# Optimization experiments

Measured on AMD Instinct MI355X. Metric: run time of the kernel, lower is better.

Reference implementation:

```python
import jax, jax.numpy as jnp
import numpy as np

N_ATOM_FEATS = 64
N_RBF = 10
N_CONV = 3
N_HIDDEN = 64
N_NODES = 50000
N_EDGES = 800000
N_GRAPHS = 512


def setup_inputs() -> dict:
    key = jax.random.key(0)
    ks = jax.random.split(key, 32)
    d = {}
    d["x_ids"] = jax.random.randint(ks[0], (N_NODES,), 0, 95)
    d["edge_index"] = jax.random.randint(ks[1], (2, N_EDGES), 0, N_NODES)
    d["edge_attr"] = jax.random.uniform(ks[2], (N_EDGES,), jnp.float32) * 6.0  # distances in [0,6)
    d["batch"] = jnp.sort(jax.random.randint(ks[3], (N_NODES,), 0, N_GRAPHS))
    # parameters
    def lin(k, fan_in, shape):
        return jax.random.normal(k, shape, jnp.float32) / np.sqrt(fan_in)
    d["emb"] = jax.random.normal(ks[4], (95, N_ATOM_FEATS), jnp.float32)
    d["blk_W1"] = lin(ks[5], N_ATOM_FEATS, (N_CONV, N_ATOM_FEATS, N_ATOM_FEATS))
    d["blk_b1"] = jnp.zeros((N_CONV, N_ATOM_FEATS), jnp.float32)
    d["blk_We"] = lin(ks[6], N_RBF, (N_CONV, N_RBF, N_ATOM_FEATS))
    d["blk_be"] = jnp.zeros((N_CONV, N_ATOM_FEATS), jnp.float32)
    d["blk_W2"] = lin(ks[7], N_ATOM_FEATS, (N_CONV, N_ATOM_FEATS, N_ATOM_FEATS))
    d["blk_b2"] = jnp.zeros((N_CONV, N_ATOM_FEATS), jnp.float32)
    d["Ws"] = lin(ks[8], N_ATOM_FEATS, (N_ATOM_FEATS, 2 * N_HIDDEN))
    d["bs"] = jnp.zeros((2 * N_HIDDEN,), jnp.float32)
    d["Wbg1"] = lin(ks[9], 2 * N_HIDDEN, (2 * N_HIDDEN, N_HIDDEN))
    d["bbg1"] = jnp.zeros((N_HIDDEN,), jnp.float32)
    d["Wbg2"] = lin(ks[10], N_HIDDEN, (N_HIDDEN, 1))
    d["bbg2"] = jnp.zeros((1,), jnp.float32)
    d["Weh1"] = lin(ks[11], 2 * N_HIDDEN, (2 * N_HIDDEN, N_HIDDEN))
    d["beh1"] = jnp.zeros((N_HIDDEN,), jnp.float32)
    d["Weh2"] = lin(ks[12], N_HIDDEN, (N_HIDDEN, 1))
    d["beh2"] = jnp.zeros((1,), jnp.float32)
    return d


def reference(x_ids, edge_index, edge_attr, batch, emb,
              blk_W1, blk_b1, blk_We, blk_be, blk_W2, blk_b2,
              Ws, bs, Wbg1, bbg1, Wbg2, bbg2, Weh1, beh1, Weh2, beh2):
    src, dst = edge_index[0], edge_index[1]
    # embedding lookup [N, F]
    x = emb[x_ids]
    # Gaussian smearing RBF: [E, n_rbf]
    offset = jnp.linspace(0.0, 6.0, N_RBF).astype(edge_attr.dtype)
    coeff = -0.5 / (offset[1] - offset[0]) ** 2
    e = jnp.exp(coeff * (edge_attr[:, None] - offset) ** 2)
    # interaction blocks (SchNet-style CFConv with residual)
    for i in range(N_CONV):
        h = x @ blk_W1[i] + blk_b1[i]                     # [N, F]
        f = e @ blk_We[i] + blk_be[i]                     # [E, F] edge filters
        m = h[src] * f                                    # [E, F] messages
        agg = jax.ops.segment_sum(m, dst, num_segments=N_NODES)
        x = x + agg @ blk_W2[i] + blk_b2[i]
        x = jax.nn.softplus(x)
    # global mean pool over graphs
    sums = jax.ops.segment_sum(x, batch, num_segments=N_GRAPHS)
    cnts = jax.ops.segment_sum(jnp.ones((x.shape[0],), x.dtype), batch, num_segments=N_GRAPHS)
    c = sums / jnp.maximum(cnts, 1.0)[:, None]
    c = jax.nn.relu(c @ Ws + bs)                          # [G, 2H]
    out_bg = jax.nn.relu(c @ Wbg1 + bbg1) @ Wbg2 + bbg2   # [G, 1]
    out_eh = jax.nn.relu(c @ Weh1 + beh1) @ Weh2 + beh2   # [G, 1]
    return (out_bg, out_eh)
```

## Files before the change

kernel.cpp:

```cpp
#include <hip/hip_runtime.h>
#include <hip/hip_fp16.h>
#include <cstddef>


__device__ __forceinline__ float softplusf(float v) {
    return fmaxf(v, 0.0f) + log1pf(__expf(-fabsf(v)));
}

#define RBF_C0 1.0f
#define RBF_C1 0.60653065971f
#define RBF_C2 0.13533528324f
#define RBF_C3 0.011108996538f
#define RBF_C4 3.3546262790e-4f
#define RBF_C5 3.7266531720e-6f
#define RBF_C6 1.5229979745e-8f
#define RBF_C7 2.2897348457e-11f
#define RBF_C8 1.2664165549e-14f
#define RBF_C9 2.5767043600e-18f

__global__ void k_hist(const int* __restrict__ dst, int* __restrict__ deg, int n_edges) {
    int e = blockIdx.x * blockDim.x + threadIdx.x;
    if (e < n_edges) atomicAdd(&deg[dst[e]], 1);
}

__global__ void k_scan1(const int* __restrict__ deg, int* __restrict__ bsum, int n) {
    __shared__ int s[256];
    int i = blockIdx.x * 256 + threadIdx.x;
    s[threadIdx.x] = (i < n) ? deg[i] : 0;
    __syncthreads();
    for (int off = 128; off > 0; off >>= 1) {
        if (threadIdx.x < off) s[threadIdx.x] += s[threadIdx.x + off];
        __syncthreads();
    }
    if (threadIdx.x == 0) bsum[blockIdx.x] = s[0];
}

__global__ void k_scan2(int* __restrict__ bsum, int nb) {
    __shared__ int s[256];
    int v = (threadIdx.x < nb) ? bsum[threadIdx.x] : 0;
    s[threadIdx.x] = v;
    __syncthreads();
    for (int off = 1; off < 256; off <<= 1) {
        int t = (threadIdx.x >= off) ? s[threadIdx.x - off] : 0;
        __syncthreads();
        s[threadIdx.x] += t;
        __syncthreads();
    }
    if (threadIdx.x < nb) bsum[threadIdx.x] = s[threadIdx.x] - v;
}

__global__ void k_scan3(const int* __restrict__ deg, const int* __restrict__ bsum,
                        int* __restrict__ off_, int* __restrict__ cursor, int n) {
    __shared__ int s[256];
    int i = blockIdx.x * 256 + threadIdx.x;
    int v = (i < n) ? deg[i] : 0;
    s[threadIdx.x] = v;
    __syncthreads();
    for (int off = 1; off < 256; off <<= 1) {
        int t = (threadIdx.x >= off) ? s[threadIdx.x - off] : 0;
        __syncthreads();
        s[threadIdx.x] += t;
        __syncthreads();
    }
    if (i < n) {
        int incl = bsum[blockIdx.x] + s[threadIdx.x];
        off_[i + 1] = incl;
        cursor[i] = incl - v;
    }
    if (i == 0) off_[0] = 0;
}

__global__ void k_scatter(const int* __restrict__ src, const int* __restrict__ dst,
                          const float* __restrict__ dist, int* __restrict__ cursor,
                          int2* __restrict__ psort, int n_edges) {
    int e = blockIdx.x * blockDim.x + threadIdx.x;
    if (e >= n_edges) return;
    int t = dst[e];
    int pos = atomicAdd(&cursor[t], 1);
    psort[pos] = make_int2(src[e], __float_as_int(dist[e]));
}

__global__ void k_gemm0(const int* __restrict__ ids, const float* __restrict__ emb,
                        const float* __restrict__ W, const float* __restrict__ bias,
                        float* __restrict__ x, __half* __restrict__ h, int n_nodes) {
    int lane = threadIdx.x & 63;
    int gw = (blockIdx.x * blockDim.x + threadIdx.x) >> 6;
    gw = __builtin_amdgcn_readfirstlane(gw);
    int nw = (gridDim.x * blockDim.x) >> 6;

    float w[64];
#pragma unroll
    for (int k = 0; k < 64; ++k) w[k] = W[k * 64 + lane];
    float bj = bias[lane];

    for (int n = gw; n < n_nodes; n += nw) {
        int id = __builtin_amdgcn_readfirstlane(ids[n]);
        const float4* xr = (const float4*)(emb + (size_t)id * 64);
        float a0 = bj, a1 = 0.f, a2 = 0.f, a3 = 0.f;
#pragma unroll
        for (int q = 0; q < 4; ++q) {
            float4 v0 = xr[4 * q + 0], v1 = xr[4 * q + 1];
            float4 v2 = xr[4 * q + 2], v3 = xr[4 * q + 3];
            a0 = fmaf(v0.x, w[16 * q + 0], a0);  a0 = fmaf(v0.y, w[16 * q + 1], a0);
            a0 = fmaf(v0.z, w[16 * q + 2], a0);  a0 = fmaf(v0.w, w[16 * q + 3], a0);
            a1 = fmaf(v1.x, w[16 * q + 4], a1);  a1 = fmaf(v1.y, w[16 * q + 5], a1);
            a1 = fmaf(v1.z, w[16 * q + 6], a1);  a1 = fmaf(v1.w, w[16 * q + 7], a1);
            a2 = fmaf(v2.x, w[16 * q + 8], a2);  a2 = fmaf(v2.y, w[16 * q + 9], a2);
            a2 = fmaf(v2.z, w[16 * q + 10], a2); a2 = fmaf(v2.w, w[16 * q + 11], a2);
            a3 = fmaf(v3.x, w[16 * q + 12], a3); a3 = fmaf(v3.y, w[16 * q + 13], a3);
            a3 = fmaf(v3.z, w[16 * q + 14], a3); a3 = fmaf(v3.w, w[16 * q + 15], a3);
        }
        x[(size_t)n * 64 + lane] = emb[(size_t)id * 64 + lane];
        h[(size_t)n * 64 + lane] = __float2half((a0 + a1) + (a2 + a3));
    }
}

__global__ void k_gemm64(const float* __restrict__ X, const float* __restrict__ W,
                         const float* __restrict__ bias, __half* __restrict__ Y, int n_nodes) {
    int lane = threadIdx.x & 63;
    int gw = (blockIdx.x * blockDim.x + threadIdx.x) >> 6;
    gw = __builtin_amdgcn_readfirstlane(gw);
    int nw = (gridDim.x * blockDim.x) >> 6;

    float w[64];
#pragma unroll
    for (int k = 0; k < 64; ++k) w[k] = W[k * 64 + lane];
    float bj = bias[lane];

    for (int n = gw; n < n_nodes; n += nw) {
        const float4* xr = (const float4*)(X + (size_t)n * 64);
        float a0 = bj, a1 = 0.f, a2 = 0.f, a3 = 0.f;
#pragma unroll
        for (int q = 0; q < 4; ++q) {
            float4 v0 = xr[4 * q + 0], v1 = xr[4 * q + 1];
            float4 v2 = xr[4 * q + 2], v3 = xr[4 * q + 3];
            a0 = fmaf(v0.x, w[16 * q + 0], a0);  a0 = fmaf(v0.y, w[16 * q + 1], a0);
            a0 = fmaf(v0.z, w[16 * q + 2], a0);  a0 = fmaf(v0.w, w[16 * q + 3], a0);
            a1 = fmaf(v1.x, w[16 * q + 4], a1);  a1 = fmaf(v1.y, w[16 * q + 5], a1);
            a1 = fmaf(v1.z, w[16 * q + 6], a1);  a1 = fmaf(v1.w, w[16 * q + 7], a1);
            a2 = fmaf(v2.x, w[16 * q + 8], a2);  a2 = fmaf(v2.y, w[16 * q + 9], a2);
            a2 = fmaf(v2.z, w[16 * q + 10], a2); a2 = fmaf(v2.w, w[16 * q + 11], a2);
            a3 = fmaf(v3.x, w[16 * q + 12], a3); a3 = fmaf(v3.y, w[16 * q + 13], a3);
            a3 = fmaf(v3.z, w[16 * q + 14], a3); a3 = fmaf(v3.w, w[16 * q + 15], a3);
        }
        Y[(size_t)n * 64 + lane] = __float2half((a0 + a1) + (a2 + a3));
    }
}

__device__ __forceinline__ float filt_d(const float wp[10], float bj, float d) {
    float A = __expf(-1.125f * d * d);
    float B = __expf(1.5f * d);
    float P = wp[9];
    P = fmaf(B, P, wp[8]); P = fmaf(B, P, wp[7]); P = fmaf(B, P, wp[6]);
    P = fmaf(B, P, wp[5]); P = fmaf(B, P, wp[4]); P = fmaf(B, P, wp[3]);
    P = fmaf(B, P, wp[2]); P = fmaf(B, P, wp[1]); P = fmaf(B, P, wp[0]);
    return fmaf(A, P, bj);
}

__global__ void k_conv(const int2* __restrict__ psort, const int* __restrict__ off,
                       const __half* __restrict__ h,
                       const float* __restrict__ We, const float* __restrict__ be,
                       const float* __restrict__ W2, const float* __restrict__ b2,
                       float* __restrict__ x, int n_nodes) {
    int lane = threadIdx.x & 63;
    int gw = (blockIdx.x * blockDim.x + threadIdx.x) >> 6;
    gw = __builtin_amdgcn_readfirstlane(gw);
    int nw = (gridDim.x * blockDim.x) >> 6;

    const float C[10] = {RBF_C0, RBF_C1, RBF_C2, RBF_C3, RBF_C4,
                         RBF_C5, RBF_C6, RBF_C7, RBF_C8, RBF_C9};
    float wp[10];
#pragma unroll
    for (int r = 0; r < 10; ++r) wp[r] = We[r * 64 + lane] * C[r];
    float bj = be[lane];
    float b2j = b2[lane];

    for (int n = gw; n < n_nodes; n += nw) {
        int k0 = off[n], k1 = off[n + 1];
        float acc = 0.0f;
        int k = k0;
        for (; k + 8 <= k1; k += 8) {
            int2 p0 = psort[k + 0], p1 = psort[k + 1], p2 = psort[k + 2], p3 = psort[k + 3];
            int2 p4 = psort[k + 4], p5 = psort[k + 5], p6 = psort[k + 6], p7 = psort[k + 7];
            float g0 = __half2float(h[(size_t)p0.x * 64 + lane]);
            float g1 = __half2float(h[(size_t)p1.x * 64 + lane]);
            float g2 = __half2float(h[(size_t)p2.x * 64 + lane]);
            float g3 = __half2float(h[(size_t)p3.x * 64 + lane]);
            float g4 = __half2float(h[(size_t)p4.x * 64 + lane]);
            float g5 = __half2float(h[(size_t)p5.x * 64 + lane]);
            float g6 = __half2float(h[(size_t)p6.x * 64 + lane]);
            float g7 = __half2float(h[(size_t)p7.x * 64 + lane]);
            acc = fmaf(g0, filt_d(wp, bj, __int_as_float(p0.y)), acc);
            acc = fmaf(g1, filt_d(wp, bj, __int_as_float(p1.y)), acc);
            acc = fmaf(g2, filt_d(wp, bj, __int_as_float(p2.y)), acc);
            acc = fmaf(g3, filt_d(wp, bj, __int_as_float(p3.y)), acc);
            acc = fmaf(g4, filt_d(wp, bj, __int_as_float(p4.y)), acc);
            acc = fmaf(g5, filt_d(wp, bj, __int_as_float(p5.y)), acc);
            acc = fmaf(g6, filt_d(wp, bj, __int_as_float(p6.y)), acc);
            acc = fmaf(g7, filt_d(wp, bj, __int_as_float(p7.y)), acc);
        }
        for (; k + 4 <= k1; k += 4) {
            int2 p0 = psort[k + 0], p1 = psort[k + 1], p2 = psort[k + 2], p3 = psort[k + 3];
            float g0 = __half2float(h[(size_t)p0.x * 64 + lane]);
            float g1 = __half2float(h[(size_t)p1.x * 64 + lane]);
            float g2 = __half2float(h[(size_t)p2.x * 64 + lane]);
            float g3 = __half2float(h[(size_t)p3.x * 64 + lane]);
            acc = fmaf(g0, filt_d(wp, bj, __int_as_float(p0.y)), acc);
            acc = fmaf(g1, filt_d(wp, bj, __int_as_float(p1.y)), acc);
            acc = fmaf(g2, filt_d(wp, bj, __int_as_float(p2.y)), acc);
            acc = fmaf(g3, filt_d(wp, bj, __int_as_float(p3.y)), acc);
        }
        for (; k < k1; ++k) {
            int2 p = psort[k];
            float g = __half2float(h[(size_t)p.x * 64 + lane]);
            acc = fmaf(g, filt_d(wp, bj, __int_as_float(p.y)), acc);
        }
        float o = b2j + x[(size_t)n * 64 + lane];
#pragma unroll 8
        for (int kk = 0; kk < 64; ++kk)
            o = fmaf(__shfl(acc, kk), W2[kk * 64 + lane], o);
        x[(size_t)n * 64 + lane] = softplusf(o);
    }
}

__global__ void k_gstart(const int* __restrict__ batch, int* __restrict__ gstart,
                         int n_nodes, int n_graphs) {
    int n = blockIdx.x * blockDim.x + threadIdx.x;
    if (n >= n_nodes) return;
    int b = batch[n];
    int prev = (n == 0) ? -1 : batch[n - 1];
    for (int g = prev + 1; g <= b; ++g) gstart[g] = n;
    if (n == n_nodes - 1)
        for (int g = b + 1; g <= n_graphs; ++g) gstart[g] = n_nodes;
}

__global__ void k_pool2(const float* __restrict__ x, const int* __restrict__ gstart,
                        float* __restrict__ c, int n_graphs) {
    __shared__ float red[256];
    int g = blockIdx.x;
    int t = threadIdx.x, j = t & 63, part = t >> 6;
    int s0 = gstart[g], s1 = gstart[g + 1];
    float acc = 0.0f;
    for (int n = s0 + part; n < s1; n += 4) acc += x[(size_t)n * 64 + j];
    red[t] = acc;
    __syncthreads();
    if (part == 0) {
        float v = red[j] + red[64 + j] + red[128 + j] + red[192 + j];
        float cnt = (float)(s1 - s0);
        c[(size_t)g * 64 + j] = v / fmaxf(cnt, 1.0f);
    }
}

__global__ void k_head(const float* __restrict__ cmean,
                       const float* __restrict__ Ws, const float* __restrict__ bs,
                       const float* __restrict__ Wbg1, const float* __restrict__ bbg1,
                       const float* __restrict__ Wbg2, const float* __restrict__ bbg2,
                       const float* __restrict__ Weh1, const float* __restrict__ beh1,
                       const float* __restrict__ Weh2, const float* __restrict__ beh2,
                       float* __restrict__ out, int n_graphs) {
    __shared__ float c[64];
    __shared__ float h1[128];
    int g = blockIdx.x;
    int t = threadIdx.x;
    if (t < 64) c[t] = cmean[(size_t)g * 64 + t];
    __syncthreads();
    float a = bs[t];
#pragma unroll 8
    for (int k = 0; k < 64; ++k) a = fmaf(c[k], Ws[k * 128 + t], a);
    h1[t] = fmaxf(a, 0.0f);
    __syncthreads();

    const float* W1p = (t < 64) ? Wbg1 : Weh1;
    const float* b1p = (t < 64) ? bbg1 : beh1;
    const float* W2p = (t < 64) ? Wbg2 : Weh2;
    float b2v = (t < 64) ? bbg2[0] : beh2[0];
    int lane = t & 63;
    float a2 = b1p[lane];
#pragma unroll 8
    for (int k = 0; k < 128; ++k) a2 = fmaf(h1[k], W1p[k * 64 + lane], a2);
    a2 = fmaxf(a2, 0.0f);
    float p = a2 * W2p[lane];
#pragma unroll
    for (int off = 32; off > 0; off >>= 1) p += __shfl_down(p, off);
    if (lane == 0) out[(t < 64 ? 0 : n_graphs) + g] = p + b2v;
}

extern "C" void kernel_launch(void* const* d_in, const int* in_sizes, int n_in,
                              void* d_out, int out_size, void* d_ws, size_t ws_size,
                              hipStream_t stream) {
    const int*   x_ids = (const int*)d_in[0];
    const int*   eidx  = (const int*)d_in[1];
    const float* eattr = (const float*)d_in[2];
    const int*   batch = (const int*)d_in[3];
    const float* emb   = (const float*)d_in[4];
    const float* W1    = (const float*)d_in[5];
    const float* b1    = (const float*)d_in[6];
    const float* We    = (const float*)d_in[7];
    const float* be    = (const float*)d_in[8];
    const float* W2    = (const float*)d_in[9];
    const float* b2    = (const float*)d_in[10];
    const float* Ws_   = (const float*)d_in[11];
    const float* bs_   = (const float*)d_in[12];
    const float* Wbg1  = (const float*)d_in[13];
    const float* bbg1  = (const float*)d_in[14];
    const float* Wbg2  = (const float*)d_in[15];
    const float* bbg2  = (const float*)d_in[16];
    const float* Weh1  = (const float*)d_in[17];
    const float* beh1  = (const float*)d_in[18];
    const float* Weh2  = (const float*)d_in[19];
    const float* beh2  = (const float*)d_in[20];

    int n_nodes  = in_sizes[0];
    int n_edges  = in_sizes[2];
    int n_graphs = out_size / 2;
    const int* src = eidx;
    const int* dst = eidx + n_edges;

    char* p = (char*)d_ws;
    float* x     = (float*)p;            p += (size_t)n_nodes * 64 * sizeof(float);
    __half* h    = (__half*)p;           p += (size_t)n_nodes * 64 * sizeof(__half);
    float* cmean = (float*)p;            p += (size_t)n_graphs * 64 * sizeof(float);
    int2* psort  = (int2*)p;             p += (size_t)n_edges * sizeof(int2);
    int* deg     = (int*)p;              p += (size_t)n_nodes * sizeof(int);
    int* off_    = (int*)p;              p += (size_t)(n_nodes + 1) * sizeof(int);
    int* cursor  = (int*)p;              p += (size_t)n_nodes * sizeof(int);
    int* bsum    = (int*)p;              p += 256 * sizeof(int);
    int* gstart  = (int*)p;              p += (size_t)(n_graphs + 1) * sizeof(int);

    float* out = (float*)d_out;

    int nb = (n_nodes + 255) / 256;

    hipMemsetAsync(deg, 0, (size_t)n_nodes * sizeof(int), stream);
    k_hist<<<(n_edges + 255) / 256, 256, 0, stream>>>(dst, deg, n_edges);
    k_scan1<<<nb, 256, 0, stream>>>(deg, bsum, n_nodes);
    k_scan2<<<1, 256, 0, stream>>>(bsum, nb);
    k_scan3<<<nb, 256, 0, stream>>>(deg, bsum, off_, cursor, n_nodes);
    k_scatter<<<(n_edges + 255) / 256, 256, 0, stream>>>(src, dst, eattr, cursor,
                                                         psort, n_edges);
    k_gstart<<<(n_nodes + 255) / 256, 256, 0, stream>>>(batch, gstart, n_nodes, n_graphs);

    k_gemm0<<<2048, 256, 0, stream>>>(x_ids, emb, W1, b1, x, h, n_nodes);
    for (int l = 0; l < 3; ++l) {
        if (l > 0)
            k_gemm64<<<2048, 256, 0, stream>>>(x, W1 + l * 64 * 64, b1 + l * 64, h, n_nodes);
        k_conv<<<4096, 256, 0, stream>>>(psort, off_, h,
                                         We + l * 10 * 64, be + l * 64,
                                         W2 + l * 64 * 64, b2 + l * 64, x, n_nodes);
    }

    k_pool2<<<n_graphs, 256, 0, stream>>>(x, gstart, cmean, n_graphs);
    k_head<<<n_graphs, 128, 0, stream>>>(cmean, Ws_, bs_, Wbg1, bbg1, Wbg2, bbg2,
                                         Weh1, beh1, Weh2, beh2, out, n_graphs);
}
```

Measured before the change: 452.5 us.

## Precompute RBF exponentials per edge, stage W2 in LDS, fuse setup and pool/head kernels

The edge scatter now computes the two exponentials of the RBF factorisation once per edge and stores them with a pre-shifted source offset in a 16-byte record. This removes per-layer exp work in the conv kernel at the cost of doubling the sorted-edge storage and its read traffic. The conv kernel stages W2 in shared memory and splits the W2 matvec into four accumulators. Histogram and graph-start computation are merged into one kernel, pool and head are merged into another, and the scan is restructured. Launch bounds and the GEMM grid sizes also change.

```diff
diff --git a/kernel.cpp b/kernel.cpp
--- a/kernel.cpp
+++ b/kernel.cpp
@@ -2,10 +2,6 @@
 #include <hip/hip_fp16.h>
 #include <cstddef>
 
-
-__device__ __forceinline__ float softplusf(float v) {
-    return fmaxf(v, 0.0f) + log1pf(__expf(-fabsf(v)));
-}
 
 #define RBF_C0 1.0f
 #define RBF_C1 0.60653065971f
@@ -18,26 +14,56 @@
 #define RBF_C8 1.2664165549e-14f
 #define RBF_C9 2.5767043600e-18f
 
-__global__ void k_hist(const int* __restrict__ dst, int* __restrict__ deg, int n_edges) {
-    int e = blockIdx.x * blockDim.x + threadIdx.x;
-    if (e < n_edges) atomicAdd(&deg[dst[e]], 1);
-}
-
-__global__ void k_scan1(const int* __restrict__ deg, int* __restrict__ bsum, int n) {
+__device__ __forceinline__ float softplusf(float v) {
+    return fmaxf(v, 0.0f) + log1pf(__expf(-fabsf(v)));
+}
+
+__device__ __forceinline__ float row_gemv(const float4* __restrict__ xr,
+                                          const float w[64], float bj) {
+    float a0 = bj, a1 = 0.f, a2 = 0.f, a3 = 0.f;
+#pragma unroll
+    for (int q = 0; q < 4; ++q) {
+        float4 v0 = xr[4 * q + 0], v1 = xr[4 * q + 1];
+        float4 v2 = xr[4 * q + 2], v3 = xr[4 * q + 3];
+        a0 = fmaf(v0.x, w[16 * q + 0], a0);  a0 = fmaf(v0.y, w[16 * q + 1], a0);
+        a0 = fmaf(v0.z, w[16 * q + 2], a0);  a0 = fmaf(v0.w, w[16 * q + 3], a0);
+        a1 = fmaf(v1.x, w[16 * q + 4], a1);  a1 = fmaf(v1.y, w[16 * q + 5], a1);
+        a1 = fmaf(v1.z, w[16 * q + 6], a1);  a1 = fmaf(v1.w, w[16 * q + 7], a1);
+        a2 = fmaf(v2.x, w[16 * q + 8], a2);  a2 = fmaf(v2.y, w[16 * q + 9], a2);
+        a2 = fmaf(v2.z, w[16 * q + 10], a2); a2 = fmaf(v2.w, w[16 * q + 11], a2);
+        a3 = fmaf(v3.x, w[16 * q + 12], a3); a3 = fmaf(v3.y, w[16 * q + 13], a3);
+        a3 = fmaf(v3.z, w[16 * q + 14], a3); a3 = fmaf(v3.w, w[16 * q + 15], a3);
+    }
+    return (a0 + a1) + (a2 + a3);
+}
+
+__device__ __forceinline__ float filt_ab(const float wp[10], float bj, float A, float B) {
+    float P = wp[9];
+    P = fmaf(B, P, wp[8]); P = fmaf(B, P, wp[7]); P = fmaf(B, P, wp[6]);
+    P = fmaf(B, P, wp[5]); P = fmaf(B, P, wp[4]); P = fmaf(B, P, wp[3]);
+    P = fmaf(B, P, wp[2]); P = fmaf(B, P, wp[1]); P = fmaf(B, P, wp[0]);
+    return fmaf(A, P, bj);
+}
+
+__global__ void k_pre(const int* __restrict__ dst, int* __restrict__ deg,
+                      const int* __restrict__ batch, int* __restrict__ gstart,
+                      int n_edges, int n_nodes, int n_graphs) {
+    int tid = blockIdx.x * blockDim.x + threadIdx.x;
+    if (tid < n_edges) atomicAdd(&deg[dst[tid]], 1);
+    if (tid < n_nodes) {
+        int b = batch[tid];
+        int prev = (tid == 0) ? -1 : batch[tid - 1];
+        for (int g = prev + 1; g <= b; ++g) gstart[g] = tid;
+        if (tid == n_nodes - 1)
+            for (int g = b + 1; g <= n_graphs; ++g) gstart[g] = n_nodes;
+    }
+}
+
+__global__ void k_scana(const int* __restrict__ deg, int* __restrict__ off_,
+                        int* __restrict__ bsum, int n) {
     __shared__ int s[256];
     int i = blockIdx.x * 256 + threadIdx.x;
-    s[threadIdx.x] = (i < n) ? deg[i] : 0;
-    __syncthreads();
-    for (int off = 128; off > 0; off >>= 1) {
-        if (threadIdx.x < off) s[threadIdx.x] += s[threadIdx.x + off];
-        __syncthreads();
-    }
-    if (threadIdx.x == 0) bsum[blockIdx.x] = s[0];
-}
-
-__global__ void k_scan2(int* __restrict__ bsum, int nb) {
-    __shared__ int s[256];
-    int v = (threadIdx.x < nb) ? bsum[threadIdx.x] : 0;
+    int v = (i < n) ? deg[i] : 0;
     s[threadIdx.x] = v;
     __syncthreads();
     for (int off = 1; off < 256; off <<= 1) {
@@ -46,14 +72,13 @@
         s[threadIdx.x] += t;
         __syncthreads();
     }
-    if (threadIdx.x < nb) bsum[threadIdx.x] = s[threadIdx.x] - v;
-}
-
-__global__ void k_scan3(const int* __restrict__ deg, const int* __restrict__ bsum,
-                        int* __restrict__ off_, int* __restrict__ cursor, int n) {
+    if (i < n) off_[i + 1] = s[threadIdx.x];
+    if (threadIdx.x == 255) bsum[blockIdx.x] = s[255];
+}
+
+__global__ void k_scanb(int* __restrict__ bsum, int nb) {
     __shared__ int s[256];
-    int i = blockIdx.x * 256 + threadIdx.x;
-    int v = (i < n) ? deg[i] : 0;
+    int v = ((int)threadIdx.x < nb) ? bsum[threadIdx.x] : 0;
     s[threadIdx.x] = v;
     __syncthreads();
     for (int off = 1; off < 256; off <<= 1) {
@@ -62,109 +87,80 @@
         s[threadIdx.x] += t;
         __syncthreads();
     }
+    if ((int)threadIdx.x < nb) bsum[threadIdx.x] = s[threadIdx.x] - v;
+}
+
+__global__ void k_scanc(const int* __restrict__ deg, const int* __restrict__ bsum,
+                        int* __restrict__ off_, int* __restrict__ cursor, int n) {
+    int i = blockIdx.x * blockDim.x + threadIdx.x;
     if (i < n) {
-        int incl = bsum[blockIdx.x] + s[threadIdx.x];
+        int incl = off_[i + 1] + bsum[i >> 8];
         off_[i + 1] = incl;
-        cursor[i] = incl - v;
+        cursor[i] = incl - deg[i];
     }
     if (i == 0) off_[0] = 0;
 }
 
 __global__ void k_scatter(const int* __restrict__ src, const int* __restrict__ dst,
                           const float* __restrict__ dist, int* __restrict__ cursor,
-                          int2* __restrict__ psort, int n_edges) {
+                          int4* __restrict__ psort, int n_edges) {
     int e = blockIdx.x * blockDim.x + threadIdx.x;
     if (e >= n_edges) return;
     int t = dst[e];
     int pos = atomicAdd(&cursor[t], 1);
-    psort[pos] = make_int2(src[e], __float_as_int(dist[e]));
-}
-
-__global__ void k_gemm0(const int* __restrict__ ids, const float* __restrict__ emb,
-                        const float* __restrict__ W, const float* __restrict__ bias,
-                        float* __restrict__ x, __half* __restrict__ h, int n_nodes) {
+    float d = dist[e];
+    float A = __expf(-1.125f * d * d);
+    float B = __expf(1.5f * d);
+    psort[pos] = make_int4(src[e] << 6, __float_as_int(A), __float_as_int(B), 0);
+}
+
+__global__ __launch_bounds__(256, 4) void k_gemm0(
+        const int* __restrict__ ids, const float* __restrict__ emb,
+        const float* __restrict__ W, const float* __restrict__ bias,
+        float* __restrict__ x, __half* __restrict__ h, int n_nodes) {
     int lane = threadIdx.x & 63;
-    int gw = (blockIdx.x * blockDim.x + threadIdx.x) >> 6;
-    gw = __builtin_amdgcn_readfirstlane(gw);
+    int gw = __builtin_amdgcn_readfirstlane((blockIdx.x * blockDim.x + threadIdx.x) >> 6);
     int nw = (gridDim.x * blockDim.x) >> 6;
-
     float w[64];
 #pragma unroll
     for (int k = 0; k < 64; ++k) w[k] = W[k * 64 + lane];
     float bj = bias[lane];
-
     for (int n = gw; n < n_nodes; n += nw) {
         int id = __builtin_amdgcn_readfirstlane(ids[n]);
-        const float4* xr = (const float4*)(emb + (size_t)id * 64);
-        float a0 = bj, a1 = 0.f, a2 = 0.f, a3 = 0.f;
-#pragma unroll
-        for (int q = 0; q < 4; ++q) {
-            float4 v0 = xr[4 * q + 0], v1 = xr[4 * q + 1];
-            float4 v2 = xr[4 * q + 2], v3 = xr[4 * q + 3];
-            a0 = fmaf(v0.x, w[16 * q + 0], a0);  a0 = fmaf(v0.y, w[16 * q + 1], a0);
-            a0 = fmaf(v0.z, w[16 * q + 2], a0);  a0 = fmaf(v0.w, w[16 * q + 3], a0);
-            a1 = fmaf(v1.x, w[16 * q + 4], a1);  a1 = fmaf(v1.y, w[16 * q + 5], a1);
-            a1 = fmaf(v1.z, w[16 * q + 6], a1);  a1 = fmaf(v1.w, w[16 * q + 7], a1);
-            a2 = fmaf(v2.x, w[16 * q + 8], a2);  a2 = fmaf(v2.y, w[16 * q + 9], a2);
-            a2 = fmaf(v2.z, w[16 * q + 10], a2); a2 = fmaf(v2.w, w[16 * q + 11], a2);
-            a3 = fmaf(v3.x, w[16 * q + 12], a3); a3 = fmaf(v3.y, w[16 * q + 13], a3);
-            a3 = fmaf(v3.z, w[16 * q + 14], a3); a3 = fmaf(v3.w, w[16 * q + 15], a3);
-        }
-        x[(size_t)n * 64 + lane] = emb[(size_t)id * 64 + lane];
-        h[(size_t)n * 64 + lane] = __float2half((a0 + a1) + (a2 + a3));
-    }
-}
-
-__global__ void k_gemm64(const float* __restrict__ X, const float* __restrict__ W,
-                         const float* __restrict__ bias, __half* __restrict__ Y, int n_nodes) {
+        const float4* xr = (const float4*)(emb + id * 64);
+        float v = row_gemv(xr, w, bj);
+        x[n * 64 + lane] = emb[id * 64 + lane];
+        h[n * 64 + lane] = __float2half(v);
+    }
+}
+
+__global__ __launch_bounds__(256, 4) void k_gemm(
+        const float* __restrict__ X, const float* __restrict__ W,
+        const float* __restrict__ bias, __half* __restrict__ Y, int n_nodes) {
     int lane = threadIdx.x & 63;
-    int gw = (blockIdx.x * blockDim.x + threadIdx.x) >> 6;
-    gw = __builtin_amdgcn_readfirstlane(gw);
+    int gw = __builtin_amdgcn_readfirstlane((blockIdx.x * blockDim.x + threadIdx.x) >> 6);
     int nw = (gridDim.x * blockDim.x) >> 6;
-
     float w[64];
 #pragma unroll
     for (int k = 0; k < 64; ++k) w[k] = W[k * 64 + lane];
     float bj = bias[lane];
-
     for (int n = gw; n < n_nodes; n += nw) {
-        const float4* xr = (const float4*)(X + (size_t)n * 64);
-        float a0 = bj, a1 = 0.f, a2 = 0.f, a3 = 0.f;
-#pragma unroll
-        for (int q = 0; q < 4; ++q) {
-            float4 v0 = xr[4 * q + 0], v1 = xr[4 * q + 1];
-            float4 v2 = xr[4 * q + 2], v3 = xr[4 * q + 3];
-            a0 = fmaf(v0.x, w[16 * q + 0], a0);  a0 = fmaf(v0.y, w[16 * q + 1], a0);
-            a0 = fmaf(v0.z, w[16 * q + 2], a0);  a0 = fmaf(v0.w, w[16 * q + 3], a0);
-            a1 = fmaf(v1.x, w[16 * q + 4], a1);  a1 = fmaf(v1.y, w[16 * q + 5], a1);
-            a1 = fmaf(v1.z, w[16 * q + 6], a1);  a1 = fmaf(v1.w, w[16 * q + 7], a1);
-            a2 = fmaf(v2.x, w[16 * q + 8], a2);  a2 = fmaf(v2.y, w[16 * q + 9], a2);
-            a2 = fmaf(v2.z, w[16 * q + 10], a2); a2 = fmaf(v2.w, w[16 * q + 11], a2);
-            a3 = fmaf(v3.x, w[16 * q + 12], a3); a3 = fmaf(v3.y, w[16 * q + 13], a3);
-            a3 = fmaf(v3.z, w[16 * q + 14], a3); a3 = fmaf(v3.w, w[16 * q + 15], a3);
-        }
-        Y[(size_t)n * 64 + lane] = __float2half((a0 + a1) + (a2 + a3));
-    }
-}
-
-__device__ __forceinline__ float filt_d(const float wp[10], float bj, float d) {
-    float A = __expf(-1.125f * d * d);
-    float B = __expf(1.5f * d);
-    float P = wp[9];
-    P = fmaf(B, P, wp[8]); P = fmaf(B, P, wp[7]); P = fmaf(B, P, wp[6]);
-    P = fmaf(B, P, wp[5]); P = fmaf(B, P, wp[4]); P = fmaf(B, P, wp[3]);
-    P = fmaf(B, P, wp[2]); P = fmaf(B, P, wp[1]); P = fmaf(B, P, wp[0]);
-    return fmaf(A, P, bj);
-}
-
-__global__ void k_conv(const int2* __restrict__ psort, const int* __restrict__ off,
-                       const __half* __restrict__ h,
-                       const float* __restrict__ We, const float* __restrict__ be,
-                       const float* __restrict__ W2, const float* __restrict__ b2,
-                       float* __restrict__ x, int n_nodes) {
+        const float4* xr = (const float4*)(X + n * 64);
+        Y[n * 64 + lane] = __float2half(row_gemv(xr, w, bj));
+    }
+}
+
+__global__ __launch_bounds__(256, 4) void k_conv(
+        const int4* __restrict__ ps, const int* __restrict__ off,
+        const __half* __restrict__ h,
+        const float* __restrict__ We, const float* __restrict__ be,
+        const float* __restrict__ W2, const float* __restrict__ b2,
+        float* __restrict__ x, int n_nodes) {
+    __shared__ float sW2[4096];
+    for (int i = threadIdx.x; i < 4096; i += 256) sW2[i] = W2[i];
+
     int lane = threadIdx.x & 63;
-    int gw = (blockIdx.x * blockDim.x + threadIdx.x) >> 6;
-    gw = __builtin_amdgcn_readfirstlane(gw);
+    int gw = __builtin_amdgcn_readfirstlane((blockIdx.x * blockDim.x + threadIdx.x) >> 6);
     int nw = (gridDim.x * blockDim.x) >> 6;
 
     const float C[10] = {RBF_C0, RBF_C1, RBF_C2, RBF_C3, RBF_C4,
@@ -172,117 +168,106 @@
     float wp[10];
 #pragma unroll
     for (int r = 0; r < 10; ++r) wp[r] = We[r * 64 + lane] * C[r];
-    float bj = be[lane];
+    float bj  = be[lane];
     float b2j = b2[lane];
+    __syncthreads();
 
     for (int n = gw; n < n_nodes; n += nw) {
         int k0 = off[n], k1 = off[n + 1];
         float acc = 0.0f;
         int k = k0;
         for (; k + 8 <= k1; k += 8) {
-            int2 p0 = psort[k + 0], p1 = psort[k + 1], p2 = psort[k + 2], p3 = psort[k + 3];
-            int2 p4 = psort[k + 4], p5 = psort[k + 5], p6 = psort[k + 6], p7 = psort[k + 7];
-            float g0 = __half2float(h[(size_t)p0.x * 64 + lane]);
-            float g1 = __half2float(h[(size_t)p1.x * 64 + lane]);
-            float g2 = __half2float(h[(size_t)p2.x * 64 + lane]);
-            float g3 = __half2float(h[(size_t)p3.x * 64 + lane]);
-            float g4 = __half2float(h[(size_t)p4.x * 64 + lane]);
-            float g5 = __half2float(h[(size_t)p5.x * 64 + lane]);
-            float g6 = __half2float(h[(size_t)p6.x * 64 + lane]);
-            float g7 = __half2float(h[(size_t)p7.x * 64 + lane]);
-            acc = fmaf(g0, filt_d(wp, bj, __int_as_float(p0.y)), acc);
-            acc = fmaf(g1, filt_d(wp, bj, __int_as_float(p1.y)), acc);
-            acc = fmaf(g2, filt_d(wp, bj, __int_as_float(p2.y)), acc);
-            acc = fmaf(g3, filt_d(wp, bj, __int_as_float(p3.y)), acc);
-            acc = fmaf(g4, filt_d(wp, bj, __int_as_float(p4.y)), acc);
-            acc = fmaf(g5, filt_d(wp, bj, __int_as_float(p5.y)), acc);
-            acc = fmaf(g6, filt_d(wp, bj, __int_as_float(p6.y)), acc);
-            acc = fmaf(g7, filt_d(wp, bj, __int_as_float(p7.y)), acc);
+            int4 p0 = ps[k + 0], p1 = ps[k + 1], p2 = ps[k + 2], p3 = ps[k + 3];
+            int4 p4 = ps[k + 4], p5 = ps[k + 5], p6 = ps[k + 6], p7 = ps[k + 7];
+            float g0 = __half2float(h[p0.x + lane]);
+            float g1 = __half2float(h[p1.x + lane]);
+            float g2 = __half2float(h[p2.x + lane]);
+            float g3 = __half2float(h[p3.x + lane]);
+            float g4 = __half2float(h[p4.x + lane]);
+            float g5 = __half2float(h[p5.x + lane]);
+            float g6 = __half2float(h[p6.x + lane]);
+            float g7 = __half2float(h[p7.x + lane]);
+            acc = fmaf(g0, filt_ab(wp, bj, __int_as_float(p0.y), __int_as_float(p0.z)), acc);
+            acc = fmaf(g1, filt_ab(wp, bj, __int_as_float(p1.y), __int_as_float(p1.z)), acc);
+            acc = fmaf(g2, filt_ab(wp, bj, __int_as_float(p2.y), __int_as_float(p2.z)), acc);
+            acc = fmaf(g3, filt_ab(wp, bj, __int_as_float(p3.y), __int_as_float(p3.z)), acc);
+            acc = fmaf(g4, filt_ab(wp, bj, __int_as_float(p4.y), __int_as_float(p4.z)), acc);
+            acc = fmaf(g5, filt_ab(wp, bj, __int_as_float(p5.y), __int_as_float(p5.z)), acc);
+            acc = fmaf(g6, filt_ab(wp, bj, __int_as_float(p6.y), __int_as_float(p6.z)), acc);
+            acc = fmaf(g7, filt_ab(wp, bj, __int_as_float(p7.y), __int_as_float(p7.z)), acc);
         }
         for (; k + 4 <= k1; k += 4) {
-            int2 p0 = psort[k + 0], p1 = psort[k + 1], p2 = psort[k + 2], p3 = psort[k + 3];
-            float g0 = __half2float(h[(size_t)p0.x * 64 + lane]);
-            float g1 = __half2float(h[(size_t)p1.x * 64 + lane]);
-            float g2 = __half2float(h[(size_t)p2.x * 64 + lane]);
-            float g3 = __half2float(h[(size_t)p3.x * 64 + lane]);
-            acc = fmaf(g0, filt_d(wp, bj, __int_as_float(p0.y)), acc);
-            acc = fmaf(g1, filt_d(wp, bj, __int_as_float(p1.y)), acc);
-            acc = fmaf(g2, filt_d(wp, bj, __int_as_float(p2.y)), acc);
-            acc = fmaf(g3, filt_d(wp, bj, __int_as_float(p3.y)), acc);
+            int4 p0 = ps[k + 0], p1 = ps[k + 1], p2 = ps[k + 2], p3 = ps[k + 3];
+            float g0 = __half2float(h[p0.x + lane]);
+            float g1 = __half2float(h[p1.x + lane]);
+            float g2 = __half2float(h[p2.x + lane]);
+            float g3 = __half2float(h[p3.x + lane]);
+            acc = fmaf(g0, filt_ab(wp, bj, __int_as_float(p0.y), __int_as_float(p0.z)), acc);
+            acc = fmaf(g1, filt_ab(wp, bj, __int_as_float(p1.y), __int_as_float(p1.z)), acc);
+            acc = fmaf(g2, filt_ab(wp, bj, __int_as_float(p2.y), __int_as_float(p2.z)), acc);
+            acc = fmaf(g3, filt_ab(wp, bj, __int_as_float(p3.y), __int_as_float(p3.z)), acc);
         }
         for (; k < k1; ++k) {
-            int2 p = psort[k];
-            float g = __half2float(h[(size_t)p.x * 64 + lane]);
-            acc = fmaf(g, filt_d(wp, bj, __int_as_float(p.y)), acc);
+            int4 p = ps[k];
+            float g = __half2float(h[p.x + lane]);
+            acc = fmaf(g, filt_ab(wp, bj, __int_as_float(p.y), __int_as_float(p.z)), acc);
         }
-        float o = b2j + x[(size_t)n * 64 + lane];
-#pragma unroll 8
-        for (int kk = 0; kk < 64; ++kk)
-            o = fmaf(__shfl(acc, kk), W2[kk * 64 + lane], o);
-        x[(size_t)n * 64 + lane] = softplusf(o);
-    }
-}
-
-__global__ void k_gstart(const int* __restrict__ batch, int* __restrict__ gstart,
-                         int n_nodes, int n_graphs) {
-    int n = blockIdx.x * blockDim.x + threadIdx.x;
-    if (n >= n_nodes) return;
-    int b = batch[n];
-    int prev = (n == 0) ? -1 : batch[n - 1];
-    for (int g = prev + 1; g <= b; ++g) gstart[g] = n;
-    if (n == n_nodes - 1)
-        for (int g = b + 1; g <= n_graphs; ++g) gstart[g] = n_nodes;
-}
-
-__global__ void k_pool2(const float* __restrict__ x, const int* __restrict__ gstart,
-                        float* __restrict__ c, int n_graphs) {
+        float o0 = b2j + x[n * 64 + lane];
+        float o1 = 0.f, o2 = 0.f, o3 = 0.f;
+#pragma unroll 4
+        for (int kk = 0; kk < 16; ++kk) {
+            o0 = fmaf(__shfl(acc, kk),      sW2[(kk)      * 64 + lane], o0);
+            o1 = fmaf(__shfl(acc, kk + 16), sW2[(kk + 16) * 64 + lane], o1);
+            o2 = fmaf(__shfl(acc, kk + 32), sW2[(kk + 32) * 64 + lane], o2);
+            o3 = fmaf(__shfl(acc, kk + 48), sW2[(kk + 48) * 64 + lane], o3);
+        }
+        x[n * 64 + lane] = softplusf((o0 + o1) + (o2 + o3));
+    }
+}
+
+__global__ void k_poolhead(const float* __restrict__ x, const int* __restrict__ gstart,
+                           const float* __restrict__ Ws, const float* __restrict__ bs,
+                           const float* __restrict__ Wbg1, const float* __restrict__ bbg1,
+                           const float* __restrict__ Wbg2, const float* __restrict__ bbg2,
+                           const float* __restrict__ Weh1, const float* __restrict__ beh1,
+                           const float* __restrict__ Weh2, const float* __restrict__ beh2,
+                           float* __restrict__ out, int n_graphs) {
     __shared__ float red[256];
+    __shared__ float c[64];
+    __shared__ float h1[128];
     int g = blockIdx.x;
     int t = threadIdx.x, j = t & 63, part = t >> 6;
     int s0 = gstart[g], s1 = gstart[g + 1];
     float acc = 0.0f;
-    for (int n = s0 + part; n < s1; n += 4) acc += x[(size_t)n * 64 + j];
+    for (int n = s0 + part; n < s1; n += 4) acc += x[n * 64 + j];
     red[t] = acc;
     __syncthreads();
-    if (part == 0) {
-        float v = red[j] + red[64 + j] + red[128 + j] + red[192 + j];
-        float cnt = (float)(s1 - s0);
-        c[(size_t)g * 64 + j] = v / fmaxf(cnt, 1.0f);
-    }
-}
-
-__global__ void k_head(const float* __restrict__ cmean,
-                       const float* __restrict__ Ws, const float* __restrict__ bs,
-                       const float* __restrict__ Wbg1, const float* __restrict__ bbg1,
-                       const float* __restrict__ Wbg2, const float* __restrict__ bbg2,
-                       const float* __restrict__ Weh1, const float* __restrict__ beh1,
-                       const float* __restrict__ Weh2, const float* __restrict__ beh2,
-                       float* __restrict__ out, int n_graphs) {
-    __shared__ float c[64];
-    __shared__ float h1[128];
-    int g = blockIdx.x;
-    int t = threadIdx.x;
-    if (t < 64) c[t] = cmean[(size_t)g * 64 + t];
-    __syncthreads();
-    float a = bs[t];
+    if (part == 0)
+        c[j] = (red[j] + red[64 + j] + red[128 + j] + red[192 + j]) /
+               fmaxf((float)(s1 - s0), 1.0f);
+    __syncthreads();
+    if (t < 128) {
+        float av = bs[t];
 #pragma unroll 8
-    for (int k = 0; k < 64; ++k) a = fmaf(c[k], Ws[k * 128 + t], a);
-    h1[t] = fmaxf(a, 0.0f);
-    __syncthreads();
-
-    const float* W1p = (t < 64) ? Wbg1 : Weh1;
-    const float* b1p = (t < 64) ? bbg1 : beh1;
-    const float* W2p = (t < 64) ? Wbg2 : Weh2;
-    float b2v = (t < 64) ? bbg2[0] : beh2[0];
-    int lane = t & 63;
-    float a2 = b1p[lane];
+        for (int k = 0; k < 64; ++k) av = fmaf(c[k], Ws[k * 128 + t], av);
+        h1[t] = fmaxf(av, 0.0f);
+    }
+    __syncthreads();
+    if (t < 128) {
+        const float* W1p = (t < 64) ? Wbg1 : Weh1;
+        const float* b1p = (t < 64) ? bbg1 : beh1;
+        const float* W2p = (t < 64) ? Wbg2 : Weh2;
+        float b2v = (t < 64) ? bbg2[0] : beh2[0];
+        int ln = t & 63;
+        float a2 = b1p[ln];
 #pragma unroll 8
-    for (int k = 0; k < 128; ++k) a2 = fmaf(h1[k], W1p[k * 64 + lane], a2);
-    a2 = fmaxf(a2, 0.0f);
-    float p = a2 * W2p[lane];
-#pragma unroll
-    for (int off = 32; off > 0; off >>= 1) p += __shfl_down(p, off);
-    if (lane == 0) out[(t < 64 ? 0 : n_graphs) + g] = p + b2v;
+        for (int k = 0; k < 128; ++k) a2 = fmaf(h1[k], W1p[k * 64 + ln], a2);
+        a2 = fmaxf(a2, 0.0f);
+        float pr = a2 * W2p[ln];
+#pragma unroll
+        for (int off = 32; off > 0; off >>= 1) pr += __shfl_down(pr, off);
+        if (ln == 0) out[(t < 64 ? 0 : n_graphs) + g] = pr + b2v;
+    }
 }
 
 extern "C" void kernel_launch(void* const* d_in, const int* in_sizes, int n_in,
@@ -317,39 +302,36 @@
     const int* dst = eidx + n_edges;
 
     char* p = (char*)d_ws;
-    float* x     = (float*)p;            p += (size_t)n_nodes * 64 * sizeof(float);
-    __half* h    = (__half*)p;           p += (size_t)n_nodes * 64 * sizeof(__half);
-    float* cmean = (float*)p;            p += (size_t)n_graphs * 64 * sizeof(float);
-    int2* psort  = (int2*)p;             p += (size_t)n_edges * sizeof(int2);
-    int* deg     = (int*)p;              p += (size_t)n_nodes * sizeof(int);
-    int* off_    = (int*)p;              p += (size_t)(n_nodes + 1) * sizeof(int);
-    int* cursor  = (int*)p;              p += (size_t)n_nodes * sizeof(int);
-    int* bsum    = (int*)p;              p += 256 * sizeof(int);
-    int* gstart  = (int*)p;              p += (size_t)(n_graphs + 1) * sizeof(int);
-
-    float* out = (float*)d_out;
-
-    int nb = (n_nodes + 255) / 256;
+    float* x     = (float*)p;   p += (size_t)n_nodes * 64 * sizeof(float);
+    __half* h    = (__half*)p;  p += (size_t)n_nodes * 64 * sizeof(__half);
+    int4* psort  = (int4*)p;    p += (size_t)n_edges * sizeof(int4);
+    int* deg     = (int*)p;     p += (size_t)n_nodes * sizeof(int);
+    int* off_    = (int*)p;     p += (size_t)(n_nodes + 1) * sizeof(int);
+    int* cursor  = (int*)p;     p += (size_t)n_nodes * sizeof(int);
+    int* bsum    = (int*)p;     p += 256 * sizeof(int);
+    int* gstart  = (int*)p;     p += (size_t)(n_graphs + 1) * sizeof(int);
+    float* out   = (float*)d_out;
+
+    int nchunks = (n_nodes + 255) / 256;
+    int nbE = (n_edges + 255) / 256;
+    int nbN = (n_nodes + 255) / 256;
+    int nbPre = (nbE > nbN) ? nbE : nbN;
 
     hipMemsetAsync(deg, 0, (size_t)n_nodes * sizeof(int), stream);
-    k_hist<<<(n_edges + 255) / 256, 256, 0, stream>>>(dst, deg, n_edges);
-    k_scan1<<<nb, 256, 0, stream>>>(deg, bsum, n_nodes);
-    k_scan2<<<1, 256, 0, stream>>>(bsum, nb);
-    k_scan3<<<nb, 256, 0, stream>>>(deg, bsum, off_, cursor, n_nodes);
-    k_scatter<<<(n_edges + 255) / 256, 256, 0, stream>>>(src, dst, eattr, cursor,
-                                                         psort, n_edges);
-    k_gstart<<<(n_nodes + 255) / 256, 256, 0, stream>>>(batch, gstart, n_nodes, n_graphs);
-
-    k_gemm0<<<2048, 256, 0, stream>>>(x_ids, emb, W1, b1, x, h, n_nodes);
+    k_pre<<<nbPre, 256, 0, stream>>>(dst, deg, batch, gstart, n_edges, n_nodes, n_graphs);
+    k_scana<<<nchunks, 256, 0, stream>>>(deg, off_, bsum, n_nodes);
+    k_scanb<<<1, 256, 0, stream>>>(bsum, nchunks);
+    k_scanc<<<nbN, 256, 0, stream>>>(deg, bsum, off_, cursor, n_nodes);
+    k_scatter<<<nbE, 256, 0, stream>>>(src, dst, eattr, cursor, psort, n_edges);
+
+    k_gemm0<<<1024, 256, 0, stream>>>(x_ids, emb, W1, b1, x, h, n_nodes);
     for (int l = 0; l < 3; ++l) {
         if (l > 0)
-            k_gemm64<<<2048, 256, 0, stream>>>(x, W1 + l * 64 * 64, b1 + l * 64, h, n_nodes);
+            k_gemm<<<1024, 256, 0, stream>>>(x, W1 + l * 4096, b1 + l * 64, h, n_nodes);
         k_conv<<<4096, 256, 0, stream>>>(psort, off_, h,
-                                         We + l * 10 * 64, be + l * 64,
-                                         W2 + l * 64 * 64, b2 + l * 64, x, n_nodes);
-    }
-
-    k_pool2<<<n_graphs, 256, 0, stream>>>(x, gstart, cmean, n_graphs);
-    k_head<<<n_graphs, 128, 0, stream>>>(cmean, Ws_, bs_, Wbg1, bbg1, Wbg2, bbg2,
-                                         Weh1, beh1, Weh2, beh2, out, n_graphs);
-}
+                                         We + l * 640, be + l * 64,
+                                         W2 + l * 4096, b2 + l * 64, x, n_nodes);
+    }
+    k_poolhead<<<n_graphs, 256, 0, stream>>>(x, gstart, Ws_, bs_, Wbg1, bbg1, Wbg2, bbg2,
+                                             Weh1, beh1, Weh2, beh2, out, n_graphs);
+}
```

After: 479.4 us. 1.06x slower.
